# Optimization experiments

Measured on AMD Instinct MI355X. Metric: run time of the kernel, lower is better.

The kernel has to match this reference:

```python
import jax, jax.numpy as jnp
import numpy as np

B, S, T = 128, 512, 256


def setup_inputs() -> dict:
    key = jax.random.key(0)
    k1, k2, k3, k4 = jax.random.split(key, 4)
    emissions = jax.random.normal(k1, (B, S, T), dtype=jnp.float32)
    mask = jnp.ones((B, S), dtype=bool)
    transitions = jax.random.normal(k2, (T, T), dtype=jnp.float32)
    start_transitions = jax.random.normal(k3, (T,), dtype=jnp.float32)
    end_transitions = jax.random.normal(k4, (T,), dtype=jnp.float32)
    return {
        "emissions": emissions,
        "mask": mask,
        "transitions": transitions,
        "start_transitions": start_transitions,
        "end_transitions": end_transitions,
    }


def reference(emissions, mask, transitions, start_transitions, end_transitions):
    """Batched Viterbi decode. Returns (paths [B,S] int32, best_scores [B] f32).

    Faithful to CRFLayer._viterbi_decode: score_0 = start + em_0; at each step
    next[i,j] = score[i] + trans[i,j] + em_t[j], take max/argmax over i; add
    end_transitions at the end; backtrack via backpointers. Masked (padded)
    steps carry score through unchanged with identity backpointers, so padded
    tail positions replicate the last valid tag (mask is all-ones here, so
    output equals the original's full-length paths).
    """
    Bn, Sn, Tn = emissions.shape
    ident = jnp.arange(Tn, dtype=jnp.int32)
    score0 = start_transitions[None, :] + emissions[:, 0]  # [B,T]

    em_ts = jnp.swapaxes(emissions, 0, 1)[1:]  # [S-1,B,T]
    m_ts = jnp.swapaxes(mask, 0, 1)[1:]        # [S-1,B]

    def step(score, inp):
        em_t, m_t = inp
        # nxt[b,i,j] = score[b,i] + trans[i,j] + em_t[b,j]
        nxt = score[:, :, None] + transitions[None, :, :] + em_t[:, None, :]
        best = jnp.max(nxt, axis=1)                    # [B,T]
        idx = jnp.argmax(nxt, axis=1).astype(jnp.int32)  # [B,T] best prev tag
        m = m_t[:, None]
        new_score = jnp.where(m, best, score)
        bp = jnp.where(m, idx, ident[None, :])
        return new_score, bp

    final_score, history = jax.lax.scan(step, score0, (em_ts, m_ts))  # history [S-1,B,T]
    final_score = final_score + end_transitions[None, :]
    best_scores = jnp.max(final_score, axis=1)                         # [B]
    last_tag = jnp.argmax(final_score, axis=1).astype(jnp.int32)       # [B]

    def back(tag, hist_t):
        prev = jnp.take_along_axis(hist_t, tag[:, None], axis=1)[:, 0]
        return prev, tag  # carry prev tag, emit current tag

    first_tag, tags_rest = jax.lax.scan(back, last_tag, history, reverse=True)
    # tags_rest[t] = tag at position t+1; first_tag = tag at position 0
    paths = jnp.concatenate([first_tag[:, None], jnp.swapaxes(tags_rest, 0, 1)], axis=1)
    return paths, best_scores
```

## Files before the change

kernel.cpp:

```cpp
#include <hip/hip_runtime.h>

#define Bn 128
#define Sn 512
#define Tn 256

typedef float v4f __attribute__((ext_vector_type(4)));

template <int CTRL>
__device__ __forceinline__ float dpp_fmax(float v) {
  int x = __builtin_amdgcn_mov_dpp(__float_as_int(v), CTRL, 0xF, 0xF, true);
  return fmaxf(v, __int_as_float(x));
}
__device__ __forceinline__ float row_fmax16(float v) {
  v = dpp_fmax<0x128>(v);
  v = dpp_fmax<0x124>(v);
  v = dpp_fmax<0x122>(v);
  v = dpp_fmax<0x121>(v);
  return v;
}
__device__ __forceinline__ float wave_fmax64(float v) {
  v = row_fmax16(v);
  int x = __builtin_amdgcn_ds_swizzle(__float_as_int(v), 0x401F);
  v = fmaxf(v, __int_as_float(x));
  v = fmaxf(v, __shfl_xor(v, 32));
  return v;
}
__device__ __forceinline__ float readlane_f(float v, int l) {
  return __int_as_float(__builtin_amdgcn_readlane(__float_as_int(v), l));
}
__device__ __forceinline__ float sel4(v4f v, int c) {
  return (c == 0) ? v.x : (c == 1) ? v.y : (c == 2) ? v.z : v.w;
}

__global__ __launch_bounds__(256) void transpose_kernel(
    const float* __restrict__ tr, float* __restrict__ trT) {
  int idx = blockIdx.x * 256 + threadIdx.x;
  int i = idx >> 8;
  int j = idx & 255;
  trT[j * Tn + i] = tr[i * Tn + j];
}

__global__ __launch_bounds__(1024, 4) void viterbi_fwd(
    const float* __restrict__ em,
    const float* __restrict__ trans,
    const float* __restrict__ start,
    float* __restrict__ scores)
{
  const int b    = blockIdx.x;
  const int tid  = threadIdx.x;
  const int lane = tid & 63;
  const int w    = tid >> 6;
  const int ip   = lane >> 2;
  const int jq   = lane & 3;
  const int jbase = w * 16 + jq * 4;
  const int i0    = ip * 16;
  const int b2 = (lane >> 2) & 1;
  const int b3 = (lane >> 3) & 1;
  const int myc = jbase + b2 * 2 + b3;
  const bool writer = (lane & 48) == 0;

  __shared__ float sbuf[2][Tn];

  float4 tr[16];
#pragma unroll
  for (int k = 0; k < 16; ++k)
    tr[k] = *reinterpret_cast<const float4*>(trans + (i0 + k) * Tn + jbase);

  const float* emb = em + (size_t)b * Sn * Tn;
  float* scb = scores + (size_t)b * Sn * Tn;

  if (tid < 64) {
    int j4 = tid * 4;
    float4 st = *reinterpret_cast<const float4*>(start + j4);
    float4 e0 = *reinterpret_cast<const float4*>(emb + j4);
    float4 s0 = make_float4(st.x + e0.x, st.y + e0.y, st.z + e0.z, st.w + e0.w);
    *reinterpret_cast<float4*>(&sbuf[0][j4]) = s0;
    *reinterpret_cast<float4*>(scb + j4) = s0;
  }

  const float* em_pre = emb + 2 * Tn + myc;
  float*       sc_w   = scb + Tn + myc;
  float e_cur = 0.0f;
  if (writer) e_cur = emb[Tn + myc];
  __syncthreads();

  int cur = 0;
  for (int t = 1; t < Sn; ++t) {
    const float* sp = &sbuf[cur][i0];
    float4 a0 = *reinterpret_cast<const float4*>(sp);
    float4 a1 = *reinterpret_cast<const float4*>(sp + 4);
    float4 a2 = *reinterpret_cast<const float4*>(sp + 8);
    float4 a3 = *reinterpret_cast<const float4*>(sp + 12);

    float e_nxt = 0.0f;
    if (writer) {
      const float* p = (t + 1 < Sn) ? em_pre : em_pre - Tn;
      e_nxt = *p;
    }

    float se[16] = {a0.x,a0.y,a0.z,a0.w, a1.x,a1.y,a1.z,a1.w,
                    a2.x,a2.y,a2.z,a2.w, a3.x,a3.y,a3.z,a3.w};

    float m0 = fmaxf(fmaxf(se[0]+tr[0].x, se[1]+tr[1].x), se[2]+tr[2].x);
    float m1 = fmaxf(fmaxf(se[0]+tr[0].y, se[1]+tr[1].y), se[2]+tr[2].y);
    float m2 = fmaxf(fmaxf(se[0]+tr[0].z, se[1]+tr[1].z), se[2]+tr[2].z);
    float m3 = fmaxf(fmaxf(se[0]+tr[0].w, se[1]+tr[1].w), se[2]+tr[2].w);
#pragma unroll
    for (int k = 3; k < 15; k += 2) {
      m0 = fmaxf(fmaxf(m0, se[k]+tr[k].x), se[k+1]+tr[k+1].x);
      m1 = fmaxf(fmaxf(m1, se[k]+tr[k].y), se[k+1]+tr[k+1].y);
      m2 = fmaxf(fmaxf(m2, se[k]+tr[k].z), se[k+1]+tr[k+1].z);
      m3 = fmaxf(fmaxf(m3, se[k]+tr[k].w), se[k+1]+tr[k+1].w);
    }
    m0 = fmaxf(m0, se[15]+tr[15].x);
    m1 = fmaxf(m1, se[15]+tr[15].y);
    m2 = fmaxf(m2, se[15]+tr[15].z);
    m3 = fmaxf(m3, se[15]+tr[15].w);

    float sA = b2 ? m0 : m2;
    float rA = __shfl_xor(sA, 4);
    float sB = b2 ? m1 : m3;
    float rB = __shfl_xor(sB, 4);
    float p0 = fmaxf(b2 ? m2 : m0, rA);
    float p1 = fmaxf(b2 ? m3 : m1, rB);
    float sC = b3 ? p0 : p1;
    float rC = __shfl_xor(sC, 8);
    float q  = fmaxf(b3 ? p1 : p0, rC);
    q = fmaxf(q, __shfl_xor(q, 16));
    q = fmaxf(q, __shfl_xor(q, 32));

    if (writer) {
      float ns = q + e_cur;
      sbuf[cur ^ 1][myc] = ns;
      *sc_w = ns;
    }
    e_cur = e_nxt;
    em_pre += Tn;
    sc_w   += Tn;
    cur ^= 1;
    __syncthreads();
  }
}

__global__ __launch_bounds__(128, 1) void viterbi_bwd(
    const float* __restrict__ em,
    const float* __restrict__ trT,
    const float* __restrict__ endt,
    const float* __restrict__ scores,
    float* __restrict__ out)
{
  const int b = blockIdx.x;
  const int tid = threadIdx.x;
  const int lane = tid & 63;
  const float* scb = scores + (size_t)b * Sn * Tn;
  const float* emb = em + (size_t)b * Sn * Tn;
  const int base = lane * 4;
  const int BIG = 1 << 30;

  __shared__ unsigned char pbuf[Sn];
  __shared__ int done;

  if (tid == 0) done = 0;
  __syncthreads();

  if (tid < 64) {
    float4 s = *reinterpret_cast<const float4*>(scb + (size_t)(Sn - 1) * Tn + base);
    float4 e = *reinterpret_cast<const float4*>(endt + base);
    float d0 = s.x + e.x;
    float d1 = s.y + e.y;
    float d2 = s.z + e.z;
    float d3 = s.w + e.w;
    float bv = fmaxf(fmaxf(fmaxf(d0, d1), d2), d3);
    bv = wave_fmax64(bv);
    int li = BIG;
    if (d3 == bv) li = base + 3;
    if (d2 == bv) li = base + 2;
    if (d1 == bv) li = base + 1;
    if (d0 == bv) li = base;
    unsigned long long mk = __ballot(li != BIG);
    int tag = __shfl(li, (int)__ffsll((long long)mk) - 1);
    if (lane == 0) {
      out[Bn * Sn + b] = bv;
      pbuf[Sn - 1] = (unsigned char)tag;
    }
    tag = __builtin_amdgcn_readfirstlane(tag);

    #define LD_V4(ptr) __builtin_nontemporal_load(reinterpret_cast<const v4f*>(ptr))

    v4f S0, S1, S2, S3, E0, E1, E2, E3;
    S3 = LD_V4(scb + (size_t)(Sn - 1) * Tn + base);
    E3 = LD_V4(emb + (size_t)(Sn - 1) * Tn + base);
    S2 = LD_V4(scb + (size_t)(Sn - 2) * Tn + base);
    E2 = LD_V4(emb + (size_t)(Sn - 2) * Tn + base);
    S1 = LD_V4(scb + (size_t)(Sn - 3) * Tn + base);
    E1 = LD_V4(emb + (size_t)(Sn - 3) * Tn + base);

    #define BWD_STEP(kk_, SP_, SC_, SN_, EP_, EN_) {                           \
      const int k_ = (kk_);                                                    \
                      \
      float4 tv = *reinterpret_cast<const float4*>(trT + (size_t)tag * Tn + base); \
      __builtin_amdgcn_sched_barrier(0);                                       \
              \
      int kp_ = (k_ >= 2) ? k_ - 2 : 0;                                        \
      SN_ = LD_V4(scb + (size_t)kp_ * Tn + base);                              \
      EN_ = LD_V4(emb + (size_t)kp_ * Tn + base);                              \
      __builtin_amdgcn_sched_barrier(0);                                       \
                    \
      int comp_ = tag & 3;                                                     \
      float dmax_ = readlane_f(sel4(SP_, comp_), tag >> 2);                    \
      float ev_   = readlane_f(sel4(EP_, comp_), tag >> 2);                    \
         \
      float c0_ = (SC_.x + tv.x) + ev_;                                        \
      float c1_ = (SC_.y + tv.y) + ev_;                                        \
      float c2_ = (SC_.z + tv.z) + ev_;                                        \
      float c3_ = (SC_.w + tv.w) + ev_;                                        \
      unsigned long long m0_ = __ballot(c0_ == dmax_);                         \
      unsigned long long m1_ = __ballot(c1_ == dmax_);                         \
      unsigned long long m2_ = __ballot(c2_ == dmax_);                         \
      unsigned long long m3_ = __ballot(c3_ == dmax_);                         \
      int f0_ = (int)__ffsll((long long)m0_);                                  \
      int f1_ = (int)__ffsll((long long)m1_);                                  \
      int f2_ = (int)__ffsll((long long)m2_);                                  \
      int f3_ = (int)__ffsll((long long)m3_);                                  \
      int i0_ = f0_ ? ((f0_ - 1) * 4 + 0) : BIG;                               \
      int i1_ = f1_ ? ((f1_ - 1) * 4 + 1) : BIG;                               \
      int i2_ = f2_ ? ((f2_ - 1) * 4 + 2) : BIG;                               \
      int i3_ = f3_ ? ((f3_ - 1) * 4 + 3) : BIG;                               \
      int ta_ = (i0_ < i1_) ? i0_ : i1_;                                       \
      int tb_ = (i2_ < i3_) ? i2_ : i3_;                                       \
      tag = (ta_ < tb_) ? ta_ : tb_;                                           \
      tag = __builtin_amdgcn_readfirstlane(tag);                               \
      if (lane == 0) pbuf[k_] = (unsigned char)tag;                            \
    }

    for (int kk = Sn - 2; kk >= 3; kk -= 4) {
      BWD_STEP(kk,     S3, S2, S0, E3, E0);
      BWD_STEP(kk - 1, S2, S1, S3, E2, E3);
      BWD_STEP(kk - 2, S1, S0, S2, E1, E2);
      BWD_STEP(kk - 3, S0, S3, S1, E0, E1);
    }
    BWD_STEP(2, S3, S2, S0, E3, E0);
    BWD_STEP(1, S2, S1, S3, E2, E3);
    BWD_STEP(0, S1, S0, S2, E1, E2);

    #undef BWD_STEP
    #undef LD_V4

    __threadfence_block();
    *(volatile int*)&done = 1;
  } else {
    volatile int* dp = &done;
    const int wbase = lane * 4;
    int off = wbase;
    while (true) {
      #pragma unroll
      for (int c = 0; c < 2; ++c) {
        float4 w0 = *reinterpret_cast<const float4*>(trT + off);
        float4 w1 = *reinterpret_cast<const float4*>(trT + off + 256);
        float4 w2 = *reinterpret_cast<const float4*>(trT + off + 512);
        float4 w3 = *reinterpret_cast<const float4*>(trT + off + 768);
        asm volatile("" :: "v"(w0.x), "v"(w1.x), "v"(w2.x), "v"(w3.x));
        off += 1024;
        if (off >= Tn * Tn) off = wbase;
      }
      if (*dp != 0) break;
    }
  }

  __syncthreads();
  if (tid < 64)
    for (int s2 = lane; s2 < Sn; s2 += 64)
      out[(size_t)b * Sn + s2] = (float)pbuf[s2];
}

extern "C" void kernel_launch(void* const* d_in, const int* in_sizes, int n_in,
                              void* d_out, int out_size, void* d_ws, size_t ws_size,
                              hipStream_t stream) {
  const float* em    = (const float*)d_in[0];
  const float* trans = (const float*)d_in[2];
  const float* start = (const float*)d_in[3];
  const float* endt  = (const float*)d_in[4];
  float* out = (float*)d_out;

  float* scores = (float*)d_ws;
  float* trT = (float*)((char*)d_ws + (size_t)Bn * Sn * Tn * 4);

  transpose_kernel<<<Tn * Tn / 256, 256, 0, stream>>>(trans, trT);
  viterbi_fwd<<<Bn, 1024, 0, stream>>>(em, trans, start, scores);
  viterbi_bwd<<<Bn, 128, 0, stream>>>(em, trT, endt, scores, out);
}
```

Baseline: 624.8 us.

## Stage backward-pass score/emission rows through an LDS ring filled by producer wave

The backtrack kernel gains a dedicated producer wavefront that prefetches score and emission rows eight at a time into a 16-deep shared-memory ring. The serial backtrack wave reads from LDS instead of issuing global loads per step, and the two waves coordinate through progress counters in shared memory. Wave priorities are set, and the cache-warming wave for the transposed transitions now sweeps once and sleeps between sweeps. The aim is to take global-load latency off the serial dependency chain, at the cost of spin-wait synchronization and a risk of stalls if the producer falls behind.

Measured after the change: 648.5 us. 3.8% more time.

```diff
diff --git a/kernel.cpp b/kernel.cpp
--- a/kernel.cpp
+++ b/kernel.cpp
@@ -142,7 +142,7 @@
   }
 }
 
-__global__ __launch_bounds__(128, 1) void viterbi_bwd(
+__global__ __launch_bounds__(192, 1) void viterbi_bwd(
     const float* __restrict__ em,
     const float* __restrict__ trT,
     const float* __restrict__ endt,
@@ -151,19 +151,26 @@
 {
   const int b = blockIdx.x;
   const int tid = threadIdx.x;
+  const int wid = tid >> 6;
   const int lane = tid & 63;
   const float* scb = scores + (size_t)b * Sn * Tn;
   const float* emb = em + (size_t)b * Sn * Tn;
   const int base = lane * 4;
   const int BIG = 1 << 30;
 
+  __shared__ float sc_ring[16][Tn];
+  __shared__ float em_ring[16][Tn];
   __shared__ unsigned char pbuf[Sn];
+  __shared__ int prog_f;
+  __shared__ int prog_k;
   __shared__ int done;
 
-  if (tid == 0) done = 0;
+  if (tid == 0) { prog_f = 0; prog_k = Sn - 1; done = 0; }
   __syncthreads();
 
-  if (tid < 64) {
+  if (wid == 0) {
+    __builtin_amdgcn_s_setprio(3);
+
     float4 s = *reinterpret_cast<const float4*>(scb + (size_t)(Sn - 1) * Tn + base);
     float4 e = *reinterpret_cast<const float4*>(endt + base);
     float d0 = s.x + e.x;
@@ -185,25 +192,27 @@
     }
     tag = __builtin_amdgcn_readfirstlane(tag);
 
-    #define LD_V4(ptr) __builtin_nontemporal_load(reinterpret_cast<const v4f*>(ptr))
-
+    #define LD_NT(ptr) __builtin_nontemporal_load(reinterpret_cast<const v4f*>(ptr))
     v4f S0, S1, S2, S3, E0, E1, E2, E3;
-    S3 = LD_V4(scb + (size_t)(Sn - 1) * Tn + base);
-    E3 = LD_V4(emb + (size_t)(Sn - 1) * Tn + base);
-    S2 = LD_V4(scb + (size_t)(Sn - 2) * Tn + base);
-    E2 = LD_V4(emb + (size_t)(Sn - 2) * Tn + base);
-    S1 = LD_V4(scb + (size_t)(Sn - 3) * Tn + base);
-    E1 = LD_V4(emb + (size_t)(Sn - 3) * Tn + base);
+    S3 = LD_NT(scb + (size_t)(Sn - 1) * Tn + base);
+    E3 = LD_NT(emb + (size_t)(Sn - 1) * Tn + base);
+    S2 = LD_NT(scb + (size_t)(Sn - 2) * Tn + base);
+    E2 = LD_NT(emb + (size_t)(Sn - 2) * Tn + base);
+    S1 = LD_NT(scb + (size_t)(Sn - 3) * Tn + base);
+    E1 = LD_NT(emb + (size_t)(Sn - 3) * Tn + base);
+    S0 = LD_NT(scb + (size_t)(Sn - 4) * Tn + base);
+    E0 = LD_NT(emb + (size_t)(Sn - 4) * Tn + base);
+    #undef LD_NT
 
     #define BWD_STEP(kk_, SP_, SC_, SN_, EP_, EN_) {                           \
       const int k_ = (kk_);                                                    \
-                      \
+              \
       float4 tv = *reinterpret_cast<const float4*>(trT + (size_t)tag * Tn + base); \
       __builtin_amdgcn_sched_barrier(0);                                       \
-              \
+                         \
       int kp_ = (k_ >= 2) ? k_ - 2 : 0;                                        \
-      SN_ = LD_V4(scb + (size_t)kp_ * Tn + base);                              \
-      EN_ = LD_V4(emb + (size_t)kp_ * Tn + base);                              \
+      SN_ = *reinterpret_cast<const v4f*>(&sc_ring[kp_ & 15][base]);           \
+      EN_ = *reinterpret_cast<const v4f*>(&em_ring[kp_ & 15][base]);           \
       __builtin_amdgcn_sched_barrier(0);                                       \
                     \
       int comp_ = tag & 3;                                                     \
@@ -234,41 +243,66 @@
     }
 
     for (int kk = Sn - 2; kk >= 3; kk -= 4) {
+      int req = 517 - kk;
+      if (req > Sn) req = Sn;
+      while (*(volatile int*)&prog_f < req) __builtin_amdgcn_s_sleep(1);
+      __asm__ volatile("" ::: "memory");
       BWD_STEP(kk,     S3, S2, S0, E3, E0);
       BWD_STEP(kk - 1, S2, S1, S3, E2, E3);
       BWD_STEP(kk - 2, S1, S0, S2, E1, E2);
       BWD_STEP(kk - 3, S0, S3, S1, E0, E1);
-    }
+      if (lane == 0) *(volatile int*)&prog_k = kk - 3;
+    }
+    while (*(volatile int*)&prog_f < Sn) __builtin_amdgcn_s_sleep(1);
+    __asm__ volatile("" ::: "memory");
     BWD_STEP(2, S3, S2, S0, E3, E0);
     BWD_STEP(1, S2, S1, S3, E2, E3);
     BWD_STEP(0, S1, S0, S2, E1, E2);
-
     #undef BWD_STEP
-    #undef LD_V4
-
-    __threadfence_block();
-    *(volatile int*)&done = 1;
+
+    __asm__ volatile("" ::: "memory");
+    if (lane == 0) *(volatile int*)&done = 1;
+
+  } else if (wid == 1) {
+    __builtin_amdgcn_s_setprio(1);
+    #define LD_NT(ptr) __builtin_nontemporal_load(reinterpret_cast<const v4f*>(ptr))
+    for (int rt = Sn - 1; rt >= 7; rt -= 8) {
+      const int rb = rt - 7;
+      while (*(volatile int*)&prog_k > rb + 17) __builtin_amdgcn_s_sleep(2);
+      __asm__ volatile("" ::: "memory");
+      v4f sbv[8], ebv[8];
+#pragma unroll
+      for (int j = 0; j < 8; ++j) {
+        int r = rt - j;
+        sbv[j] = LD_NT(scb + (size_t)r * Tn + base);
+        ebv[j] = LD_NT(emb + (size_t)r * Tn + base);
+      }
+#pragma unroll
+      for (int j = 0; j < 8; ++j) {
+        int r = rt - j;
+        *reinterpret_cast<v4f*>(&sc_ring[r & 15][base]) = sbv[j];
+        *reinterpret_cast<v4f*>(&em_ring[r & 15][base]) = ebv[j];
+      }
+      __asm__ volatile("" ::: "memory");
+      if (lane == 0) *(volatile int*)&prog_f = Sn - rb;
+    }
+    #undef LD_NT
+
   } else {
+    __builtin_amdgcn_s_setprio(0);
     volatile int* dp = &done;
-    const int wbase = lane * 4;
-    int off = wbase;
-    while (true) {
-      #pragma unroll
-      for (int c = 0; c < 2; ++c) {
+    while (*dp == 0) {
+      for (int off = base; off < Tn * Tn; off += 256) {
         float4 w0 = *reinterpret_cast<const float4*>(trT + off);
-        float4 w1 = *reinterpret_cast<const float4*>(trT + off + 256);
-        float4 w2 = *reinterpret_cast<const float4*>(trT + off + 512);
-        float4 w3 = *reinterpret_cast<const float4*>(trT + off + 768);
-        asm volatile("" :: "v"(w0.x), "v"(w1.x), "v"(w2.x), "v"(w3.x));
-        off += 1024;
-        if (off >= Tn * Tn) off = wbase;
+        asm volatile("" :: "v"(w0.x), "v"(w0.y), "v"(w0.z), "v"(w0.w));
       }
-      if (*dp != 0) break;
+      for (int z = 0; z < 6 && *dp == 0; ++z)
+        __builtin_amdgcn_s_sleep(127);
     }
   }
 
   __syncthreads();
-  if (tid < 64)
+  if (wid == 0)
     for (int s2 = lane; s2 < Sn; s2 += 64)
       out[(size_t)b * Sn + s2] = (float)pbuf[s2];
 }
@@ -287,5 +321,5 @@
 
   transpose_kernel<<<Tn * Tn / 256, 256, 0, stream>>>(trans, trT);
   viterbi_fwd<<<Bn, 1024, 0, stream>>>(em, trans, start, scores);
-  viterbi_bwd<<<Bn, 128, 0, stream>>>(em, trT, endt, scores, out);
-}
+  viterbi_bwd<<<Bn, 192, 0, stream>>>(em, trT, endt, scores, out);
+}
```
